# Optimization experiments

Measured on AMD Instinct MI355X. Metric: run time of the kernel, lower is better.

## Reference

```python
import jax, jax.numpy as jnp
import numpy as np

DIM = 384
HEADS = 12
WH, WW = 7, 7
N = WH * WW
NW = 64          # windows per image
B_ = 4096        # total windows (64 images * 64 windows)


def _relative_position_index():
    ch = np.arange(WH)
    cw = np.arange(WW)
    coords = np.stack(np.meshgrid(ch, cw, indexing='ij'))          # 2, Wh, Ww
    cf = coords.reshape(2, -1)                                     # 2, N
    rel = cf[:, :, None] - cf[:, None, :]                          # 2, N, N
    rel = rel.transpose(1, 2, 0).copy()                            # N, N, 2
    rel[:, :, 0] += WH - 1
    rel[:, :, 1] += WW - 1
    rel[:, :, 0] *= 2 * WW - 1
    return rel.sum(-1).astype(np.int32)                            # N, N


def setup_inputs() -> dict:
    key = jax.random.key(0)
    ks = jax.random.split(key, 7)
    x = jax.random.normal(ks[0], (B_, N, DIM), dtype=jnp.float32)
    mask = jax.random.normal(ks[1], (NW, N, N), dtype=jnp.float32)
    qkv_w = jax.random.normal(ks[2], (3 * DIM, DIM), dtype=jnp.float32) * 0.02
    qkv_b = jax.random.normal(ks[3], (3 * DIM,), dtype=jnp.float32) * 0.02
    proj_w = jax.random.normal(ks[4], (DIM, DIM), dtype=jnp.float32) * 0.02
    proj_b = jax.random.normal(ks[5], (DIM,), dtype=jnp.float32) * 0.02
    bias_table = jax.random.normal(ks[6], (169, HEADS), dtype=jnp.float32) * 0.02
    rel_idx = jnp.asarray(_relative_position_index())
    return {"x": x, "mask": mask, "qkv_w": qkv_w, "qkv_b": qkv_b,
            "proj_w": proj_w, "proj_b": proj_b, "bias_table": bias_table,
            "rel_idx": rel_idx}


def reference(x, mask, qkv_w, qkv_b, proj_w, proj_b, bias_table, rel_idx):
    B, Nn, C = x.shape
    hd = C // HEADS
    scale = hd ** (-0.5)
    # qkv projection: (B, N, 3C) -> (3, B, H, N, hd)
    qkv = (x @ qkv_w.T + qkv_b).reshape(B, Nn, 3, HEADS, hd).transpose(2, 0, 3, 1, 4)
    q, k, v = qkv[0], qkv[1], qkv[2]
    attn = jnp.einsum('bhnd,bhmd->bhnm', q * scale, k)             # B, H, N, N
    # gathered relative-position bias: (N, N, H) -> (H, N, N)
    bias = bias_table[rel_idx.reshape(-1)].reshape(Nn, Nn, HEADS).transpose(2, 0, 1)
    attn = attn + bias[None]
    nW = mask.shape[0]
    attn = attn.reshape(B // nW, nW, HEADS, Nn, Nn) + mask[None, :, None]
    attn = attn.reshape(B, HEADS, Nn, Nn)
    attn = jax.nn.softmax(attn, axis=-1)
    out = jnp.einsum('bhnm,bhmd->bnhd', attn, v).reshape(B, Nn, C)
    return out @ proj_w.T + proj_b
```

## Files before the change

### kernel.cpp

```cpp
#include <hip/hip_runtime.h>


#define NTOK 49
#define DIM 384
#define HEADS 12
#define QKV_OC 1152
#define QKV_ELEMS (1152*384)
#define PROJ_ELEMS (384*384)
#define CMB_ELEMS (64*12*49*49)
#define SCALE 0.17677669529663687f

typedef __attribute__((ext_vector_type(8))) __bf16 bf16x8;
typedef __attribute__((ext_vector_type(4))) float f32x4;

union BF8 { bf16x8 v; unsigned short u[8]; uint4 q; };

__device__ __forceinline__ unsigned short f2bf(float f) {
  union { float f; unsigned u; } x; x.f = f;
  unsigned r = x.u + 0x7fffu + ((x.u >> 16) & 1u);
  return (unsigned short)(r >> 16);
}

__device__ __forceinline__ bf16x8 zbf8() {
  BF8 z;
  #pragma unroll
  for (int j = 0; j < 8; ++j) z.u[j] = 0;
  return z.v;
}

__global__ void prep_kernel(const float* __restrict__ qkv_w,
                            const float* __restrict__ proj_w,
                            const float* __restrict__ bias_table,
                            const int* __restrict__ rel_idx,
                            const float* __restrict__ mask,
                            const float* __restrict__ qkv_b,
                            unsigned short* __restrict__ wq,
                            unsigned short* __restrict__ wp,
                            float* __restrict__ cmb,
                            float* __restrict__ qb2) {
  int i = blockIdx.x * 256 + threadIdx.x;
  if (i < QKV_ELEMS) {
    float v = qkv_w[i];
    if (i < 384 * 384) v *= SCALE;
    wq[i] = f2bf(v);
  } else if (i < QKV_ELEMS + PROJ_ELEMS) {
    int j = i - QKV_ELEMS;
    wp[j] = f2bf(proj_w[j]);
  } else if (i < QKV_ELEMS + PROJ_ELEMS + CMB_ELEMS) {
    int j = i - QKV_ELEMS - PROJ_ELEMS;
    int row = j % 49;
    int tok = (j / 49) % 49;
    int h   = (j / 2401) % 12;
    int wi  = j / (2401 * 12);
    cmb[j] = bias_table[rel_idx[row * 49 + tok] * HEADS + h]
           + mask[(wi * 49 + row) * 49 + tok];
  } else if (i < QKV_ELEMS + PROJ_ELEMS + CMB_ELEMS + QKV_OC) {
    int c = i - QKV_ELEMS - PROJ_ELEMS - CMB_ELEMS;
    qb2[c] = qkv_b[c] * (c < 384 ? SCALE : 1.0f);
  }
}

template<int NS, int FP32IN, int BF16OUT>
__global__ __launch_bounds__(256, 3) void gemm_full(
    const void* __restrict__ Ain, const unsigned short* __restrict__ W,
    const float* __restrict__ bias, void* __restrict__ Cout, int Mrows) {
  __shared__ alignas(16) unsigned short Bsm[64 * 384];
  const int tid = threadIdx.x;
  const int wave = tid >> 6, lane = tid & 63, g = lane >> 4, li = lane & 15;
  const int tb = blockIdx.x * 64 + wave * 16;
  const int arow = tb + li;

  bf16x8 afr[12];
  if (arow < Mrows) {
    if (FP32IN) {
      const float* ap = (const float*)Ain + (size_t)arow * 384 + g * 8;
      #pragma unroll
      for (int ks = 0; ks < 12; ++ks) {
        float4 f0 = *(const float4*)(ap + ks * 32);
        float4 f1 = *(const float4*)(ap + ks * 32 + 4);
        BF8 t;
        t.u[0] = f2bf(f0.x); t.u[1] = f2bf(f0.y); t.u[2] = f2bf(f0.z); t.u[3] = f2bf(f0.w);
        t.u[4] = f2bf(f1.x); t.u[5] = f2bf(f1.y); t.u[6] = f2bf(f1.z); t.u[7] = f2bf(f1.w);
        afr[ks] = t.v;
      }
    } else {
      const unsigned short* ap = (const unsigned short*)Ain + (size_t)arow * 384 + g * 8;
      #pragma unroll
      for (int ks = 0; ks < 12; ++ks) afr[ks] = *(const bf16x8*)(ap + ks * 32);
    }
  } else {
    bf16x8 z = zbf8();
    #pragma unroll
    for (int ks = 0; ks < 12; ++ks) afr[ks] = z;
  }

  #pragma unroll 1
  for (int ns = 0; ns < NS; ++ns) {
    if (ns) __syncthreads();
    #pragma unroll
    for (int it = 0; it < 12; ++it) {
      int gi = it * 256 + tid;
      int row = gi / 48, gcs = gi % 48;
      int gc = gcs ^ (row & 7);
      bf16x8 v = *(const bf16x8*)(W + (size_t)(ns * 64 + row) * 384 + gc * 8);
      *(bf16x8*)&Bsm[row * 384 + gcs * 8] = v;
    }
    __syncthreads();

    f32x4 acc[4];
    #pragma unroll
    for (int i = 0; i < 4; ++i) acc[i] = (f32x4){0.f, 0.f, 0.f, 0.f};
    #pragma unroll
    for (int k2 = 0; k2 < 12; ++k2) {
      #pragma unroll
      for (int nt = 0; nt < 4; ++nt) {
        int brow = nt * 16 + li;
        bf16x8 bf = *(const bf16x8*)&Bsm[brow * 384 + (((k2 * 4 + g) ^ (li & 7)) << 3)];
        acc[nt] = __builtin_amdgcn_mfma_f32_16x16x32_bf16(afr[k2], bf, acc[nt], 0, 0, 0);
      }
    }
    #pragma unroll
    for (int nt = 0; nt < 4; ++nt) {
      int col = ns * 64 + nt * 16 + li;
      float bv = bias[col];
      #pragma unroll
      for (int r4 = 0; r4 < 4; ++r4) {
        int row = tb + g * 4 + r4;
        if (row < Mrows) {
          float v = acc[nt][r4] + bv;
          if (BF16OUT) ((unsigned short*)Cout)[(size_t)row * (NS * 64) + col] = f2bf(v);
          else         ((float*)Cout)[(size_t)row * (NS * 64) + col] = v;
        }
      }
    }
  }
}

#define AT_Q 0
#define AT_K (49*384)
#define AT_V (AT_K + 49*128)
#define AT_ELEMS (AT_V + 49*138)

__global__ __launch_bounds__(512, 4) void attn_kernel(
    const unsigned short* __restrict__ qkv,
    const float* __restrict__ cmb,
    unsigned short* __restrict__ Obuf,
    int wb0) {
  __shared__ unsigned short lds[AT_ELEMS];
  const int tid  = threadIdx.x;
  const int wave = tid >> 6, lane = tid & 63;
  const int g = lane >> 4, li = lane & 15;
  const int relw = blockIdx.x;
  const int wi = (wb0 + relw) & 63;
  const size_t rowbase = (size_t)relw * 49;
  const int mgrp = wave >> 1, ng = wave & 1;
  const int arow = mgrp * 16 + li;

  #pragma unroll
  for (int it = 0; it < 5; ++it) {
    int gidx = it * 512 + tid;
    if (gidx < 2352) {
      int row = gidx / 48, gc = gidx % 48;
      bf16x8 v = *(const bf16x8*)(qkv + (rowbase + row) * 1152 + gc * 8);
      *(bf16x8*)&lds[AT_Q + row * 384 + ((gc ^ (row & 7)) << 3)] = v;
    }
  }

  #pragma unroll 1
  for (int c = 0; c < 3; ++c) {
    if (c) __syncthreads();
    #pragma unroll
    for (int it = 0; it < 2; ++it) {
      int gidx = it * 512 + tid;
      if (gidx < 784) {
        int row = gidx >> 4, gc = gidx & 15;
        bf16x8 v = *(const bf16x8*)(qkv + (rowbase + row) * 1152 + 384 + c * 128 + gc * 8);
        *(bf16x8*)&lds[AT_K + row * 128 + ((gc ^ (row & 7)) << 3)] = v;
      }
    }
    #pragma unroll
    for (int it = 0; it < 2; ++it) {
      int gidx = it * 512 + tid;
      if (gidx < 784) {
        int row = gidx >> 4, gc = gidx & 15;
        BF8 v;
        v.q = *(const uint4*)(qkv + (rowbase + row) * 1152 + 768 + c * 128 + gc * 8);
        int e = AT_V + row * 138 + gc * 8;
        *(unsigned*)&lds[e]     = v.q.x;
        *(unsigned*)&lds[e + 2] = v.q.y;
        *(unsigned*)&lds[e + 4] = v.q.z;
        *(unsigned*)&lds[e + 6] = v.q.w;
      }
    }
    __syncthreads();

    #pragma unroll 1
    for (int b = 0; b < 2; ++b) {
      const int hh = ng * 2 + b;
      const int h  = c * 4 + hh;

      bf16x8 qa = (arow < NTOK)
          ? *(const bf16x8*)&lds[AT_Q + arow * 384 + (((h * 4 + g) ^ (arow & 7)) << 3)]
          : zbf8();

      f32x4 sv[4];
      #pragma unroll
      for (int nt = 0; nt < 4; ++nt) {
        int tok = nt * 16 + li;
        bf16x8 kf = (tok < NTOK)
            ? *(const bf16x8*)&lds[AT_K + tok * 128 + (((hh * 4 + g) ^ (tok & 7)) << 3)]
            : zbf8();
        f32x4 z4 = (f32x4){0.f, 0.f, 0.f, 0.f};
        sv[nt] = __builtin_amdgcn_mfma_f32_16x16x32_bf16(kf, qa, z4, 0, 0, 0);
      }

      const float* cb = cmb + (size_t)(wi * HEADS + h) * (NTOK * NTOK);
      #pragma unroll
      for (int nt = 0; nt < 4; ++nt) {
        #pragma unroll
        for (int r4 = 0; r4 < 4; ++r4) {
          int tok = nt * 16 + g * 4 + r4;
          float v;
          if (tok < NTOK) {
            v = sv[nt][r4];
            if (arow < NTOK) v += cb[tok * NTOK + arow];
          } else {
            v = -1e30f;
          }
          sv[nt][r4] = v;
        }
      }

      float m = -1e30f;
      #pragma unroll
      for (int nt = 0; nt < 4; ++nt)
        #pragma unroll
        for (int r4 = 0; r4 < 4; ++r4) m = fmaxf(m, sv[nt][r4]);
      m = fmaxf(m, __shfl_xor(m, 16));
      m = fmaxf(m, __shfl_xor(m, 32));
      float s = 0.f;
      #pragma unroll
      for (int nt = 0; nt < 4; ++nt)
        #pragma unroll
        for (int r4 = 0; r4 < 4; ++r4) {
          float e = __expf(sv[nt][r4] - m);
          sv[nt][r4] = e;
          s += e;
        }
      s += __shfl_xor(s, 16);
      s += __shfl_xor(s, 32);
      float inv = 1.f / s;
      #pragma unroll
      for (int nt = 0; nt < 4; ++nt)
        #pragma unroll
        for (int r4 = 0; r4 < 4; ++r4) sv[nt][r4] *= inv;

      bf16x8 pa[2];
      #pragma unroll
      for (int k2 = 0; k2 < 2; ++k2) {
        BF8 pf;
        #pragma unroll
        for (int j = 0; j < 8; ++j) {
          int srcLane = (((g * 2 + (j >> 2)) & 3) << 4) | li;
          float v0 = __shfl(sv[k2 * 2][j & 3], srcLane);
          float v1 = __shfl(sv[k2 * 2 + 1][j & 3], srcLane);
          pf.u[j] = f2bf((g >= 2) ? v1 : v0);
        }
        pa[k2] = pf.v;
      }

      f32x4 oa[2];
      oa[0] = (f32x4){0.f, 0.f, 0.f, 0.f};
      oa[1] = (f32x4){0.f, 0.f, 0.f, 0.f};
      #pragma unroll
      for (int k2 = 0; k2 < 2; ++k2) {
        #pragma unroll
        for (int nt2 = 0; nt2 < 2; ++nt2) {
          BF8 vb;
          int ch = hh * 32 + nt2 * 16 + li;
          #pragma unroll
          for (int j = 0; j < 8; ++j) {
            int tok = k2 * 32 + g * 8 + j;
            vb.u[j] = (tok < NTOK) ? lds[AT_V + tok * 138 + ch] : (unsigned short)0;
          }
          oa[nt2] = __builtin_amdgcn_mfma_f32_16x16x32_bf16(pa[k2], vb.v, oa[nt2], 0, 0, 0);
        }
      }

      #pragma unroll
      for (int nt2 = 0; nt2 < 2; ++nt2) {
        int col = h * 32 + nt2 * 16 + li;
        #pragma unroll
        for (int r4 = 0; r4 < 4; ++r4) {
          int row = mgrp * 16 + g * 4 + r4;
          if (row < NTOK)
            Obuf[(rowbase + row) * 384 + col] = f2bf(oa[nt2][r4]);
        }
      }
    }
  }
}

extern "C" void kernel_launch(void* const* d_in, const int* in_sizes, int n_in,
                              void* d_out, int out_size, void* d_ws, size_t ws_size,
                              hipStream_t stream) {
  (void)in_sizes; (void)n_in; (void)out_size;
  const float* x          = (const float*)d_in[0];
  const float* mask       = (const float*)d_in[1];
  const float* qkv_w      = (const float*)d_in[2];
  const float* qkv_b      = (const float*)d_in[3];
  const float* proj_w     = (const float*)d_in[4];
  const float* proj_b     = (const float*)d_in[5];
  const float* bias_table = (const float*)d_in[6];
  const int*   rel_idx    = (const int*)d_in[7];
  float* out = (float*)d_out;

  char* ws = (char*)d_ws;
  size_t off = 0;
  unsigned short* wq  = (unsigned short*)(ws + off); off += (size_t)QKV_ELEMS * 2;
  unsigned short* wp  = (unsigned short*)(ws + off); off += (size_t)PROJ_ELEMS * 2;
  float*          qb2 = (float*)(ws + off);          off += (size_t)QKV_OC * 4;
  float*          cmb = (float*)(ws + off);          off += (size_t)CMB_ELEMS * 4;
  const size_t fixed = off;

  const int cands[7] = {1024, 2048, 512, 4096, 256, 128, 64};
  int WB = 64;
  for (int ci = 0; ci < 7; ++ci) {
    size_t need = fixed + (size_t)cands[ci] * 49 * (1152 + 384) * 2;
    if (need <= ws_size) { WB = cands[ci]; break; }
  }
  unsigned short* qkv = (unsigned short*)(ws + fixed);
  unsigned short* xb  = qkv + (size_t)WB * 49 * 1152;

  const int prep_total = QKV_ELEMS + PROJ_ELEMS + CMB_ELEMS + QKV_OC;
  prep_kernel<<<(prep_total + 255) / 256, 256, 0, stream>>>(
      qkv_w, proj_w, bias_table, rel_idx, mask, qkv_b, wq, wp, cmb, qb2);

  const int NB = 4096 / WB;
  const int Mrows = WB * 49;
  const int grid = (Mrows + 63) / 64;
  for (int b = 0; b < NB; ++b) {
    gemm_full<18, 1, 1><<<grid, 256, 0, stream>>>(
        (const void*)(x + (size_t)b * Mrows * 384), wq, qb2, (void*)qkv, Mrows);
    attn_kernel<<<WB, 512, 0, stream>>>(qkv, cmb, xb, b * WB);
    gemm_full<6, 0, 0><<<grid, 256, 0, stream>>>(
        (const void*)xb, wp, proj_b, (void*)(out + (size_t)b * Mrows * 384), Mrows);
  }
}
```

Baseline: 1.234 ms.

## Double-buffer weight tiles in GEMM with pre-swizzled weights and register staging

The weights are pre-swizzled in the prep kernel, so the GEMM can copy them into shared memory linearly, without per-element index math. The GEMM now uses two 32-column shared-memory buffers. It prefetches the next tile into registers while MFMAs run on the current one, which hides global load latency behind compute. In exchange each stage is half as wide, so there are twice as many stages and barriers, and each wave issues fewer MFMAs per B-tile load.

```diff
diff --git a/kernel.cpp b/kernel.cpp
--- a/kernel.cpp
+++ b/kernel.cpp
@@ -40,12 +40,14 @@
                             float* __restrict__ qb2) {
   int i = blockIdx.x * 256 + threadIdx.x;
   if (i < QKV_ELEMS) {
-    float v = qkv_w[i];
-    if (i < 384 * 384) v *= SCALE;
+    int c = i / 384, j = i % 384, s = j >> 3, e = j & 7;
+    float v = qkv_w[c * 384 + ((s ^ (c & 7)) << 3) + e];
+    if (c < 384) v *= SCALE;
     wq[i] = f2bf(v);
   } else if (i < QKV_ELEMS + PROJ_ELEMS) {
-    int j = i - QKV_ELEMS;
-    wp[j] = f2bf(proj_w[j]);
+    int k = i - QKV_ELEMS;
+    int c = k / 384, j = k % 384, s = j >> 3, e = j & 7;
+    wp[k] = f2bf(proj_w[c * 384 + ((s ^ (c & 7)) << 3) + e]);
   } else if (i < QKV_ELEMS + PROJ_ELEMS + CMB_ELEMS) {
     int j = i - QKV_ELEMS - PROJ_ELEMS;
     int row = j % 49;
@@ -61,14 +63,15 @@
 }
 
 template<int NS, int FP32IN, int BF16OUT>
-__global__ __launch_bounds__(256, 3) void gemm_full(
-    const void* __restrict__ Ain, const unsigned short* __restrict__ W,
+__global__ __launch_bounds__(256, 3) void gemm_pipe(
+    const void* __restrict__ Ain, const unsigned short* __restrict__ Wsw,
     const float* __restrict__ bias, void* __restrict__ Cout, int Mrows) {
-  __shared__ alignas(16) unsigned short Bsm[64 * 384];
+  __shared__ alignas(16) unsigned short Bsm[2][32 * 384];
   const int tid = threadIdx.x;
   const int wave = tid >> 6, lane = tid & 63, g = lane >> 4, li = lane & 15;
   const int tb = blockIdx.x * 64 + wave * 16;
   const int arow = tb + li;
+  const int soff = wave * 6 * 512 + lane * 8;
 
   bf16x8 afr[12];
   if (arow < Mrows) {
@@ -94,45 +97,60 @@
     for (int ks = 0; ks < 12; ++ks) afr[ks] = z;
   }
 
+  uint4 st[6];
+  {
+    const unsigned short* p = Wsw + soff;
+    #pragma unroll
+    for (int i = 0; i < 6; ++i) st[i] = *(const uint4*)(p + i * 512);
+    unsigned short* d = &Bsm[0][soff];
+    #pragma unroll
+    for (int i = 0; i < 6; ++i) *(uint4*)(d + i * 512) = st[i];
+  }
+  __syncthreads();
+
   #pragma unroll 1
   for (int ns = 0; ns < NS; ++ns) {
-    if (ns) __syncthreads();
-    #pragma unroll
-    for (int it = 0; it < 12; ++it) {
-      int gi = it * 256 + tid;
-      int row = gi / 48, gcs = gi % 48;
-      int gc = gcs ^ (row & 7);
-      bf16x8 v = *(const bf16x8*)(W + (size_t)(ns * 64 + row) * 384 + gc * 8);
-      *(bf16x8*)&Bsm[row * 384 + gcs * 8] = v;
-    }
-    __syncthreads();
-
-    f32x4 acc[4];
-    #pragma unroll
-    for (int i = 0; i < 4; ++i) acc[i] = (f32x4){0.f, 0.f, 0.f, 0.f};
+    const int cur = ns & 1;
+    if (ns + 1 < NS) {
+      const unsigned short* p = Wsw + (size_t)(ns + 1) * 12288 + soff;
+      #pragma unroll
+      for (int i = 0; i < 6; ++i) st[i] = *(const uint4*)(p + i * 512);
+    }
+
+    f32x4 acc[2];
+    acc[0] = (f32x4){0.f, 0.f, 0.f, 0.f};
+    acc[1] = (f32x4){0.f, 0.f, 0.f, 0.f};
     #pragma unroll
     for (int k2 = 0; k2 < 12; ++k2) {
       #pragma unroll
-      for (int nt = 0; nt < 4; ++nt) {
-        int brow = nt * 16 + li;
-        bf16x8 bf = *(const bf16x8*)&Bsm[brow * 384 + (((k2 * 4 + g) ^ (li & 7)) << 3)];
+      for (int nt = 0; nt < 2; ++nt) {
+        bf16x8 bf = *(const bf16x8*)&Bsm[cur][(nt * 16 + li) * 384 +
+                                             (((k2 * 4 + g) ^ (li & 7)) << 3)];
         acc[nt] = __builtin_amdgcn_mfma_f32_16x16x32_bf16(afr[k2], bf, acc[nt], 0, 0, 0);
       }
     }
-    #pragma unroll
-    for (int nt = 0; nt < 4; ++nt) {
-      int col = ns * 64 + nt * 16 + li;
+
+    #pragma unroll
+    for (int nt = 0; nt < 2; ++nt) {
+      int col = ns * 32 + nt * 16 + li;
       float bv = bias[col];
       #pragma unroll
       for (int r4 = 0; r4 < 4; ++r4) {
         int row = tb + g * 4 + r4;
         if (row < Mrows) {
           float v = acc[nt][r4] + bv;
-          if (BF16OUT) ((unsigned short*)Cout)[(size_t)row * (NS * 64) + col] = f2bf(v);
-          else         ((float*)Cout)[(size_t)row * (NS * 64) + col] = v;
-        }
-      }
-    }
+          if (BF16OUT) ((unsigned short*)Cout)[(size_t)row * (NS * 32) + col] = f2bf(v);
+          else         ((float*)Cout)[(size_t)row * (NS * 32) + col] = v;
+        }
+      }
+    }
+
+    if (ns + 1 < NS) {
+      unsigned short* d = &Bsm[cur ^ 1][soff];
+      #pragma unroll
+      for (int i = 0; i < 6; ++i) *(uint4*)(d + i * 512) = st[i];
+    }
+    __syncthreads();
   }
 }
 
@@ -340,10 +358,10 @@
   const int Mrows = WB * 49;
   const int grid = (Mrows + 63) / 64;
   for (int b = 0; b < NB; ++b) {
-    gemm_full<18, 1, 1><<<grid, 256, 0, stream>>>(
+    gemm_pipe<36, 1, 1><<<grid, 256, 0, stream>>>(
         (const void*)(x + (size_t)b * Mrows * 384), wq, qb2, (void*)qkv, Mrows);
     attn_kernel<<<WB, 512, 0, stream>>>(qkv, cmb, xb, b * WB);
-    gemm_full<6, 0, 0><<<grid, 256, 0, stream>>>(
+    gemm_pipe<12, 0, 0><<<grid, 256, 0, stream>>>(
         (const void*)xb, wp, proj_b, (void*)(out + (size_t)b * Mrows * 384), Mrows);
   }
 }
```

Result: slower. 2.203 ms (+78.6%).
